# Performance work log

Measured on AMD Instinct MI355X. Metric: run time of the kernel, lower is better.

The kernel has to match this reference:

```python
import jax, jax.numpy as jnp
import numpy as np

N_NODES = 100000


def gcn_layer(x, src, dst, W, b):
    """PyG GCNConv: add self-loops, symmetric deg normalization, XW then scatter-add."""
    n = x.shape[0]
    loop = jnp.arange(n, dtype=src.dtype)
    s = jnp.concatenate([src, loop])
    d = jnp.concatenate([dst, loop])
    # degree of target nodes (includes self-loop)
    deg = jax.ops.segment_sum(jnp.ones_like(d, dtype=x.dtype), d, num_segments=n)
    dinv = jnp.where(deg > 0, jax.lax.rsqrt(deg), 0.0)
    norm = dinv[s] * dinv[d]                      # [E+N]
    h = x @ W                                     # [N, out]
    msg = h[s] * norm[:, None]                    # [E+N, out]
    out = jax.ops.segment_sum(msg, d, num_segments=n) + b
    return out


def setup_inputs() -> dict:
    key = jax.random.key(0)
    k1, k2, k3, k4 = jax.random.split(key, 4)
    d_in, d_hid, d_out = 256, 256, 128
    E = 3200000
    x = jax.random.normal(k1, (N_NODES, d_in), dtype=jnp.float32)
    edge_index = jax.random.randint(k2, (2, E), 0, N_NODES, dtype=jnp.int64)
    # glorot-style init for GCN weights
    W1 = jax.random.normal(k3, (d_in, d_hid), dtype=jnp.float32) / np.sqrt(d_in)
    b1 = jnp.zeros((d_hid,), dtype=jnp.float32)
    W2 = jax.random.normal(k4, (d_hid, d_out), dtype=jnp.float32) / np.sqrt(d_hid)
    b2 = jnp.zeros((d_out,), dtype=jnp.float32)
    return {"x": x, "W1": W1, "b1": b1, "W2": W2, "b2": b2, "edge_index": edge_index}


def reference(x, W1, b1, W2, b2, edge_index):
    src, dst = edge_index[0], edge_index[1]
    h = jax.nn.relu(gcn_layer(x, src, dst, W1, b1))
    out = jax.nn.relu(gcn_layer(h, src, dst, W2, b2))
    return out
```

## Files before the change

kernel.cpp:

```cpp
#include <hip/hip_runtime.h>


typedef short          s16x8 __attribute__((ext_vector_type(8)));
typedef float          f32x4 __attribute__((ext_vector_type(4)));
typedef float          f32x2 __attribute__((ext_vector_type(2)));
typedef unsigned short u16x8 __attribute__((ext_vector_type(8)));
typedef unsigned short u16x4 __attribute__((ext_vector_type(4)));

__device__ __forceinline__ float bf2f(unsigned short u) {
  union { unsigned int i; float f; } x; x.i = ((unsigned int)u) << 16; return x.f;
}
__device__ __forceinline__ unsigned short f2bf(float f) {
  union { float f; unsigned int i; } x; x.f = f;
  unsigned int r = x.i + 0x7FFFu + ((x.i >> 16) & 1u);
  return (unsigned short)(r >> 16);
}
__device__ __forceinline__ void acc2(f32x2& a, unsigned int pair) {
  union { unsigned int u; float f; } lo, hi;
  lo.u = pair << 16;
  hi.u = pair & 0xFFFF0000u;
  f32x2 v = {lo.f, hi.f};
  a += v;
}


#define NBUCK_PAD 1024
#define BIN_CHUNK 32768

__global__ __launch_bounds__(256) void k_hist(const int* __restrict__ dst,
                                              int* __restrict__ bcnt, int E) {
  __shared__ int h[NBUCK_PAD];
  int t = threadIdx.x;
  for (int i = t; i < NBUCK_PAD; i += 256) h[i] = 0;
  __syncthreads();
  int n4 = E >> 2;
  int stride = gridDim.x * 256;
  const int4* d4 = (const int4*)dst;
  for (int e = blockIdx.x * 256 + t; e < n4; e += stride) {
    int4 v = d4[e];
    atomicAdd(&h[v.x >> 7], 1);
    atomicAdd(&h[v.y >> 7], 1);
    atomicAdd(&h[v.z >> 7], 1);
    atomicAdd(&h[v.w >> 7], 1);
  }
  if (blockIdx.x == 0) {
    for (int e = n4 * 4 + t; e < E; e += 256) atomicAdd(&h[dst[e] >> 7], 1);
  }
  __syncthreads();
  for (int i = t; i < NBUCK_PAD; i += 256) {
    int v = h[i];
    if (v) atomicAdd(bcnt + i, v);
  }
}

__global__ void k_bscan(const int* __restrict__ bcnt, int* __restrict__ bptr,
                        int* __restrict__ bcur, int* __restrict__ rowptr, int M, int E) {
  __shared__ int sh[NBUCK_PAD];
  int t = threadIdx.x;
  int v = bcnt[t];
  sh[t] = v; __syncthreads();
  int x = v;
  for (int off = 1; off < NBUCK_PAD; off <<= 1) {
    int y = (t >= off) ? sh[t - off] : 0;
    __syncthreads();
    x += y; sh[t] = x;
    __syncthreads();
  }
  bptr[t] = x - v;
  bcur[t] = x - v;
  if (t == NBUCK_PAD - 1) bptr[NBUCK_PAD] = x;
  if (t == 0) rowptr[M] = E;
}

__global__ __launch_bounds__(256) void k_bin(const int* __restrict__ src,
                                             const int* __restrict__ dst,
                                             int* __restrict__ bcur,
                                             unsigned int* __restrict__ binned, int E) {
  __shared__ int hist[NBUCK_PAD];
  __shared__ int base[NBUCK_PAD];
  int t = threadIdx.x;
  int e0 = blockIdx.x * BIN_CHUNK;
  int e1 = min(e0 + BIN_CHUNK, E);
  for (int i = t; i < NBUCK_PAD; i += 256) hist[i] = 0;
  __syncthreads();
  for (int e = e0 + t; e < e1; e += 256) atomicAdd(&hist[dst[e] >> 7], 1);
  __syncthreads();
  for (int i = t; i < NBUCK_PAD; i += 256) {
    int h = hist[i];
    base[i] = h ? atomicAdd(bcur + i, h) : 0;
    hist[i] = 0;
  }
  __syncthreads();
  for (int e = e0 + t; e < e1; e += 256) {
    int d = dst[e], s = src[e];
    int b = d >> 7;
    int p = base[b] + atomicAdd(&hist[b], 1);
    binned[p] = ((unsigned)(d & 127) << 17) | (unsigned)s;
  }
}

__global__ __launch_bounds__(256) void k_csr(const unsigned int* __restrict__ binned,
                                             const int* __restrict__ bptr,
                                             int* __restrict__ rowptr,
                                             float* __restrict__ dinv,
                                             int* __restrict__ col, int M) {
  __shared__ int deg[128];
  __shared__ int sc[128];
  __shared__ int cur[128];
  int b = blockIdx.x, t = threadIdx.x;
  int n0 = b << 7;
  int nn = min(128, M - n0);
  int e0 = bptr[b], e1 = bptr[b + 1];
  if (t < 128) deg[t] = 0;
  __syncthreads();
  for (int e = e0 + t; e < e1; e += 256) atomicAdd(&deg[(binned[e] >> 17) & 127], 1);
  __syncthreads();
  if (t < 128) sc[t] = deg[t];
  __syncthreads();
  for (int off = 1; off < 128; off <<= 1) {
    int y = 0;
    if (t < 128 && t >= off) y = sc[t - off];
    __syncthreads();
    if (t < 128) sc[t] += y;
    __syncthreads();
  }
  if (t < nn) {
    int excl = sc[t] - deg[t];
    rowptr[n0 + t] = e0 + excl;
    dinv[n0 + t] = rsqrtf((float)(deg[t] + 1));
    cur[t] = excl;
  }
  __syncthreads();
  for (int e = e0 + t; e < e1; e += 256) {
    unsigned v = binned[e];
    int dl = (v >> 17) & 127;
    int p = e0 + atomicAdd(&cur[dl], 1);
    col[p] = (int)(v & 0x1FFFFu);
  }
}


__global__ void k_cvt_w(const float* __restrict__ W1, const float* __restrict__ W2,
                        unsigned short* __restrict__ w1t, unsigned short* __restrict__ w2t) {
  int i = blockIdx.x * 256 + threadIdx.x;
  if (i < 256 * 256) {
    int k = i >> 8, n = i & 255;
    w1t[n * 256 + k] = f2bf(W1[i]);
  } else {
    int j = i - 256 * 256;
    if (j < 256 * 128) {
      int k = j >> 7, n = j & 127;
      w2t[n * 256 + k] = f2bf(W2[j]);
    }
  }
}


__device__ __forceinline__ int swz4(int row, int kc) { return kc ^ ((row & 3) << 3); }

__global__ __launch_bounds__(512) void k_gemm1(
    const float* __restrict__ X, const unsigned short* __restrict__ Bt,
    const float* __restrict__ dinv, unsigned short* __restrict__ G, int M) {
  const int K = 256;
  __shared__ short lA[128 * 32];
  __shared__ short lB[256 * 32];
  int tid = threadIdx.x;
  int wid = tid >> 6, lane = tid & 63;
  int wm = wid >> 2, wn = wid & 3;
  int l15 = lane & 15;
  int lkg = (lane >> 4) * 8;
  int bm = blockIdx.x * 128;

  f32x4 acc[4][4] = {};

  for (int kt = 0; kt < 8; ++kt) {
    int k0 = kt * 32;
    __syncthreads();
#pragma unroll
    for (int h = 0; h < 2; ++h) {
      int cid = tid + h * 512;
      int r = cid >> 3, c4 = (cid & 7) * 4;
      int gr = bm + r;
      float4 v = {0.f, 0.f, 0.f, 0.f};
      if (gr < M) v = *(const float4*)(X + (size_t)gr * K + k0 + c4);
      u16x4 o; o[0] = f2bf(v.x); o[1] = f2bf(v.y); o[2] = f2bf(v.z); o[3] = f2bf(v.w);
      *(u16x4*)(&lA[r * 32 + swz4(r, c4)]) = o;
    }
#pragma unroll
    for (int h = 0; h < 2; ++h) {
      int cid = tid + h * 512;
      int n = cid >> 2, kc = (cid & 3) * 8;
      s16x8 v = *(const s16x8*)(Bt + (size_t)n * K + k0 + kc);
      *(s16x8*)(&lB[n * 32 + swz4(n, kc)]) = v;
    }
    __syncthreads();

    s16x8 af[4], bfr[4];
#pragma unroll
    for (int mi = 0; mi < 4; ++mi) {
      int r = wm * 64 + mi * 16 + l15;
      af[mi] = *(const s16x8*)(&lA[r * 32 + swz4(r, lkg)]);
    }
#pragma unroll
    for (int ni = 0; ni < 4; ++ni) {
      int c = wn * 64 + ni * 16 + l15;
      bfr[ni] = *(const s16x8*)(&lB[c * 32 + swz4(c, lkg)]);
    }
#pragma unroll
    for (int mi = 0; mi < 4; ++mi)
#pragma unroll
      for (int ni = 0; ni < 4; ++ni)
        acc[mi][ni] = __builtin_amdgcn_mfma_f32_16x16x32_bf16(af[mi], bfr[ni], acc[mi][ni], 0, 0, 0);
  }

#pragma unroll
  for (int mi = 0; mi < 4; ++mi) {
    int mrow0 = bm + wm * 64 + mi * 16 + (lane >> 4) * 4;
#pragma unroll
    for (int j = 0; j < 4; ++j) {
      int m = mrow0 + j;
      if (m < M) {
        float dv = dinv[m];
#pragma unroll
        for (int ni = 0; ni < 4; ++ni)
          G[(size_t)m * 256 + wn * 64 + ni * 16 + l15] = f2bf(acc[mi][ni][j] * dv);
      }
    }
  }
}


__global__ __launch_bounds__(512) void k_gemm2(
    const unsigned short* __restrict__ A, const unsigned short* __restrict__ Bt,
    const float* __restrict__ dinv, unsigned short* __restrict__ G, int M) {
  const int K = 256;
  __shared__ short lA[128 * 32];
  __shared__ short lB[128 * 32];
  int tid = threadIdx.x;
  int wid = tid >> 6, lane = tid & 63;
  int wm = wid >> 2, wn = wid & 3;
  int l15 = lane & 15;
  int lkg = (lane >> 4) * 8;
  int bm = blockIdx.x * 128;

  f32x4 acc[4][2] = {};

  for (int kt = 0; kt < 8; ++kt) {
    int k0 = kt * 32;
    __syncthreads();
    {
      int r = tid >> 2, kc = (tid & 3) * 8;
      int gr = bm + r;
      s16x8 v = {0, 0, 0, 0, 0, 0, 0, 0};
      if (gr < M) v = *(const s16x8*)(A + (size_t)gr * K + k0 + kc);
      *(s16x8*)(&lA[r * 32 + swz4(r, kc)]) = v;
    }
    {
      int n = tid >> 2, kc = (tid & 3) * 8;
      s16x8 v = *(const s16x8*)(Bt + (size_t)n * K + k0 + kc);
      *(s16x8*)(&lB[n * 32 + swz4(n, kc)]) = v;
    }
    __syncthreads();

    s16x8 af[4], bfr[2];
#pragma unroll
    for (int mi = 0; mi < 4; ++mi) {
      int r = wm * 64 + mi * 16 + l15;
      af[mi] = *(const s16x8*)(&lA[r * 32 + swz4(r, lkg)]);
    }
#pragma unroll
    for (int ni = 0; ni < 2; ++ni) {
      int c = wn * 32 + ni * 16 + l15;
      bfr[ni] = *(const s16x8*)(&lB[c * 32 + swz4(c, lkg)]);
    }
#pragma unroll
    for (int mi = 0; mi < 4; ++mi)
#pragma unroll
      for (int ni = 0; ni < 2; ++ni)
        acc[mi][ni] = __builtin_amdgcn_mfma_f32_16x16x32_bf16(af[mi], bfr[ni], acc[mi][ni], 0, 0, 0);
  }

#pragma unroll
  for (int mi = 0; mi < 4; ++mi) {
    int mrow0 = bm + wm * 64 + mi * 16 + (lane >> 4) * 4;
#pragma unroll
    for (int j = 0; j < 4; ++j) {
      int m = mrow0 + j;
      if (m < M) {
        float dv = dinv[m];
#pragma unroll
        for (int ni = 0; ni < 2; ++ni)
          G[(size_t)m * 128 + wn * 32 + ni * 16 + l15] = f2bf(acc[mi][ni][j] * dv);
      }
    }
  }
}


__global__ __launch_bounds__(256) void k_agg256(
    const unsigned short* __restrict__ G, const int* __restrict__ rowptr,
    const int* __restrict__ col, const float* __restrict__ dinv,
    const float* __restrict__ bias, unsigned short* __restrict__ H, int M) {
  int lane = threadIdx.x & 63;
  int v = (blockIdx.x << 2) + (threadIdx.x >> 6);
  if (v >= M) return;
  int slot = lane >> 5;
  int l32 = lane & 31;
  int boff = l32 * 16;
  const char* Gb = (const char*)G;
  f32x2 a[4] = {};
  if (slot == 0) {
    uint4 w = *(const uint4*)(Gb + (((unsigned)v) << 9) + boff);
    acc2(a[0], w.x); acc2(a[1], w.y); acc2(a[2], w.z); acc2(a[3], w.w);
  }
  int jb = rowptr[v], je = rowptr[v + 1];
  int j = jb;
  for (; j + 4 <= je; j += 4) {
    unsigned u0 = (unsigned)col[j + slot];
    unsigned u1 = (unsigned)col[j + 2 + slot];
    uint4 w0 = *(const uint4*)(Gb + (u0 << 9) + boff);
    uint4 w1 = *(const uint4*)(Gb + (u1 << 9) + boff);
    acc2(a[0], w0.x); acc2(a[1], w0.y); acc2(a[2], w0.z); acc2(a[3], w0.w);
    acc2(a[0], w1.x); acc2(a[1], w1.y); acc2(a[2], w1.z); acc2(a[3], w1.w);
  }
  for (; j + 2 <= je; j += 2) {
    unsigned u = (unsigned)col[j + slot];
    uint4 w = *(const uint4*)(Gb + (u << 9) + boff);
    acc2(a[0], w.x); acc2(a[1], w.y); acc2(a[2], w.z); acc2(a[3], w.w);
  }
  if (j < je && slot == 0) {
    unsigned u = (unsigned)col[j];
    uint4 w = *(const uint4*)(Gb + (u << 9) + boff);
    acc2(a[0], w.x); acc2(a[1], w.y); acc2(a[2], w.z); acc2(a[3], w.w);
  }
#pragma unroll
  for (int k = 0; k < 4; ++k) {
    a[k].x += __shfl_xor(a[k].x, 32, 64);
    a[k].y += __shfl_xor(a[k].y, 32, 64);
  }
  if (slot == 0) {
    float dv = dinv[v];
    const float* bp = bias + l32 * 8;
    u16x8 o;
#pragma unroll
    for (int k = 0; k < 4; ++k) {
      o[2 * k]     = f2bf(fmaxf(fmaf(dv, a[k].x, bp[2 * k]),     0.f));
      o[2 * k + 1] = f2bf(fmaxf(fmaf(dv, a[k].y, bp[2 * k + 1]), 0.f));
    }
    *(u16x8*)(H + (size_t)v * 256 + l32 * 8) = o;
  }
}


__global__ __launch_bounds__(256) void k_agg128(
    const unsigned short* __restrict__ G, const int* __restrict__ rowptr,
    const int* __restrict__ col, const float* __restrict__ dinv,
    const float* __restrict__ bias, float* __restrict__ Out, int M) {
  int lane = threadIdx.x & 63;
  int v = (blockIdx.x << 2) + (threadIdx.x >> 6);
  if (v >= M) return;
  int slot = lane >> 4;
  int l16 = lane & 15;
  int boff = l16 * 16;
  const char* Gb = (const char*)G;
  f32x2 a[4] = {};
  if (slot == 0) {
    uint4 w = *(const uint4*)(Gb + (((unsigned)v) << 8) + boff);
    acc2(a[0], w.x); acc2(a[1], w.y); acc2(a[2], w.z); acc2(a[3], w.w);
  }
  int jb = rowptr[v], je = rowptr[v + 1];
  int j = jb;
  for (; j + 8 <= je; j += 8) {
    unsigned u0 = (unsigned)col[j + slot];
    unsigned u1 = (unsigned)col[j + 4 + slot];
    uint4 w0 = *(const uint4*)(Gb + (u0 << 8) + boff);
    uint4 w1 = *(const uint4*)(Gb + (u1 << 8) + boff);
    acc2(a[0], w0.x); acc2(a[1], w0.y); acc2(a[2], w0.z); acc2(a[3], w0.w);
    acc2(a[0], w1.x); acc2(a[1], w1.y); acc2(a[2], w1.z); acc2(a[3], w1.w);
  }
  for (; j + 4 <= je; j += 4) {
    unsigned u = (unsigned)col[j + slot];
    uint4 w = *(const uint4*)(Gb + (u << 8) + boff);
    acc2(a[0], w.x); acc2(a[1], w.y); acc2(a[2], w.z); acc2(a[3], w.w);
  }
  int rem = je - j;
  if (slot < rem) {
    unsigned u = (unsigned)col[j + slot];
    uint4 w = *(const uint4*)(Gb + (u << 8) + boff);
    acc2(a[0], w.x); acc2(a[1], w.y); acc2(a[2], w.z); acc2(a[3], w.w);
  }
#pragma unroll
  for (int k = 0; k < 4; ++k) {
    a[k].x += __shfl_xor(a[k].x, 16, 64);
    a[k].y += __shfl_xor(a[k].y, 16, 64);
    a[k].x += __shfl_xor(a[k].x, 32, 64);
    a[k].y += __shfl_xor(a[k].y, 32, 64);
  }
  if (slot == 0) {
    float dv = dinv[v];
    const float* bp = bias + l16 * 8;
    float4 r0, r1;
    r0.x = fmaxf(fmaf(dv, a[0].x, bp[0]), 0.f);
    r0.y = fmaxf(fmaf(dv, a[0].y, bp[1]), 0.f);
    r0.z = fmaxf(fmaf(dv, a[1].x, bp[2]), 0.f);
    r0.w = fmaxf(fmaf(dv, a[1].y, bp[3]), 0.f);
    r1.x = fmaxf(fmaf(dv, a[2].x, bp[4]), 0.f);
    r1.y = fmaxf(fmaf(dv, a[2].y, bp[5]), 0.f);
    r1.z = fmaxf(fmaf(dv, a[3].x, bp[6]), 0.f);
    r1.w = fmaxf(fmaf(dv, a[3].y, bp[7]), 0.f);
    float* op = Out + (size_t)v * 128 + l16 * 8;
    *(float4*)op = r0;
    *(float4*)(op + 4) = r1;
  }
}


extern "C" void kernel_launch(void* const* d_in, const int* in_sizes, int n_in,
                              void* d_out, int out_size, void* d_ws, size_t ws_size,
                              hipStream_t stream) {
  const float* x  = (const float*)d_in[0];
  const float* W1 = (const float*)d_in[1];
  const float* b1 = (const float*)d_in[2];
  const float* W2 = (const float*)d_in[3];
  const float* b2 = (const float*)d_in[4];
  const int*   ei = (const int*)d_in[5];

  const int D_IN = 256, D_HID = 256, D_OUT = 128;
  const int M = in_sizes[0] / D_IN;
  const int E = in_sizes[5] / 2;
  const int* src = ei;
  const int* dst = ei + E;

  char* p = (char*)d_ws;
  auto alloc = [&](size_t bytes) { void* r = (void*)p; p += (bytes + 255) & ~(size_t)255; return r; };
  float* dinv = (float*)alloc((size_t)M * 4);
  int* rowptr = (int*)alloc((size_t)(M + 1) * 4);
  int* bcnt   = (int*)alloc(NBUCK_PAD * 4);
  int* bptr   = (int*)alloc((NBUCK_PAD + 1) * 4);
  int* bcur   = (int*)alloc(NBUCK_PAD * 4);
  int* colx   = (int*)alloc((size_t)E * 4);
  unsigned short* w1t = (unsigned short*)alloc((size_t)D_HID * D_IN * 2);
  unsigned short* w2t = (unsigned short*)alloc((size_t)D_OUT * D_HID * 2);
  unsigned short* g1  = (unsigned short*)alloc((size_t)M * D_HID * 2);
  unsigned short* hid = (unsigned short*)alloc((size_t)M * D_HID * 2);
  unsigned short* g2  = (unsigned short*)alloc((size_t)M * D_OUT * 2);
  unsigned int* binned = (unsigned int*)g1;

  int nbuck = (M + 127) >> 7;
  int nbin  = (E + BIN_CHUNK - 1) / BIN_CHUNK;
  int nb4   = (M + 3) / 4;

  hipMemsetAsync(bcnt, 0, NBUCK_PAD * 4, stream);
  k_hist <<<104, 256, 0, stream>>>(dst, bcnt, E);
  k_bscan<<<1, NBUCK_PAD, 0, stream>>>(bcnt, bptr, bcur, rowptr, M, E);
  k_bin  <<<nbin, 256, 0, stream>>>(src, dst, bcur, binned, E);
  k_csr  <<<nbuck, 256, 0, stream>>>(binned, bptr, rowptr, dinv, colx, M);

  k_cvt_w<<<(256 * 256 + 256 * 128 + 255) / 256, 256, 0, stream>>>(W1, W2, w1t, w2t);

  k_gemm1 <<<nbuck, 512, 0, stream>>>(x, w1t, dinv, g1, M);
  k_agg256<<<nb4, 256, 0, stream>>>(g1, rowptr, colx, dinv, b1, hid, M);
  k_gemm2 <<<nbuck, 512, 0, stream>>>(hid, w2t, dinv, g2, M);
  k_agg128<<<nb4, 256, 0, stream>>>(g2, rowptr, colx, dinv, b2, (float*)d_out, M);
}
```

Baseline: 552.1 us.

## Shrink GEMM tiles to 64 rows, add nontemporal memory ops, smaller bin chunk

Both GEMMs now use 64-row tiles with 256-thread blocks and a 2x2 wave layout, each wave covering more output columns. This doubles the grid size for better occupancy across CUs. Streaming loads of column indices and stores of GEMM/aggregation outputs now use nontemporal hints to limit cache pollution, and the edge binning chunk is reduced so more blocks are launched. Risks: the B tile is reloaded more often per output row, and the nontemporal stores may evict data the next kernel wants to read from cache.

```diff
diff --git a/kernel.cpp b/kernel.cpp
--- a/kernel.cpp
+++ b/kernel.cpp
@@ -25,7 +25,7 @@
 
 
 #define NBUCK_PAD 1024
-#define BIN_CHUNK 32768
+#define BIN_CHUNK 8192
 
 __global__ __launch_bounds__(256) void k_hist(const int* __restrict__ dst,
                                               int* __restrict__ bcnt, int E) {
@@ -158,27 +158,27 @@
 
 __device__ __forceinline__ int swz4(int row, int kc) { return kc ^ ((row & 3) << 3); }
 
-__global__ __launch_bounds__(512) void k_gemm1(
+__global__ __launch_bounds__(256) void k_gemm1(
     const float* __restrict__ X, const unsigned short* __restrict__ Bt,
     const float* __restrict__ dinv, unsigned short* __restrict__ G, int M) {
   const int K = 256;
-  __shared__ short lA[128 * 32];
+  __shared__ short lA[64 * 32];
   __shared__ short lB[256 * 32];
   int tid = threadIdx.x;
   int wid = tid >> 6, lane = tid & 63;
-  int wm = wid >> 2, wn = wid & 3;
+  int wm = wid >> 1, wn = wid & 1;
   int l15 = lane & 15;
   int lkg = (lane >> 4) * 8;
-  int bm = blockIdx.x * 128;
-
-  f32x4 acc[4][4] = {};
+  int bm = blockIdx.x * 64;
+
+  f32x4 acc[2][8] = {};
 
   for (int kt = 0; kt < 8; ++kt) {
     int k0 = kt * 32;
     __syncthreads();
 #pragma unroll
     for (int h = 0; h < 2; ++h) {
-      int cid = tid + h * 512;
+      int cid = tid + h * 256;
       int r = cid >> 3, c4 = (cid & 7) * 4;
       int gr = bm + r;
       float4 v = {0.f, 0.f, 0.f, 0.f};
@@ -187,63 +187,64 @@
       *(u16x4*)(&lA[r * 32 + swz4(r, c4)]) = o;
     }
 #pragma unroll
-    for (int h = 0; h < 2; ++h) {
-      int cid = tid + h * 512;
+    for (int h = 0; h < 4; ++h) {
+      int cid = tid + h * 256;
       int n = cid >> 2, kc = (cid & 3) * 8;
       s16x8 v = *(const s16x8*)(Bt + (size_t)n * K + k0 + kc);
       *(s16x8*)(&lB[n * 32 + swz4(n, kc)]) = v;
     }
     __syncthreads();
 
-    s16x8 af[4], bfr[4];
-#pragma unroll
-    for (int mi = 0; mi < 4; ++mi) {
-      int r = wm * 64 + mi * 16 + l15;
+    s16x8 af[2], bfr[8];
+#pragma unroll
+    for (int mi = 0; mi < 2; ++mi) {
+      int r = wm * 32 + mi * 16 + l15;
       af[mi] = *(const s16x8*)(&lA[r * 32 + swz4(r, lkg)]);
     }
 #pragma unroll
-    for (int ni = 0; ni < 4; ++ni) {
-      int c = wn * 64 + ni * 16 + l15;
+    for (int ni = 0; ni < 8; ++ni) {
+      int c = wn * 128 + ni * 16 + l15;
       bfr[ni] = *(const s16x8*)(&lB[c * 32 + swz4(c, lkg)]);
     }
 #pragma unroll
-    for (int mi = 0; mi < 4; ++mi)
-#pragma unroll
-      for (int ni = 0; ni < 4; ++ni)
+    for (int mi = 0; mi < 2; ++mi)
+#pragma unroll
+      for (int ni = 0; ni < 8; ++ni)
         acc[mi][ni] = __builtin_amdgcn_mfma_f32_16x16x32_bf16(af[mi], bfr[ni], acc[mi][ni], 0, 0, 0);
   }
 
 #pragma unroll
-  for (int mi = 0; mi < 4; ++mi) {
-    int mrow0 = bm + wm * 64 + mi * 16 + (lane >> 4) * 4;
+  for (int mi = 0; mi < 2; ++mi) {
+    int mrow0 = bm + wm * 32 + mi * 16 + (lane >> 4) * 4;
 #pragma unroll
     for (int j = 0; j < 4; ++j) {
       int m = mrow0 + j;
       if (m < M) {
         float dv = dinv[m];
 #pragma unroll
-        for (int ni = 0; ni < 4; ++ni)
-          G[(size_t)m * 256 + wn * 64 + ni * 16 + l15] = f2bf(acc[mi][ni][j] * dv);
+        for (int ni = 0; ni < 8; ++ni)
+          __builtin_nontemporal_store(f2bf(acc[mi][ni][j] * dv),
+                                      G + (size_t)m * 256 + wn * 128 + ni * 16 + l15);
       }
     }
   }
 }
 
 
-__global__ __launch_bounds__(512) void k_gemm2(
+__global__ __launch_bounds__(256) void k_gemm2(
     const unsigned short* __restrict__ A, const unsigned short* __restrict__ Bt,
     const float* __restrict__ dinv, unsigned short* __restrict__ G, int M) {
   const int K = 256;
-  __shared__ short lA[128 * 32];
+  __shared__ short lA[64 * 32];
   __shared__ short lB[128 * 32];
   int tid = threadIdx.x;
   int wid = tid >> 6, lane = tid & 63;
-  int wm = wid >> 2, wn = wid & 3;
+  int wm = wid >> 1, wn = wid & 1;
   int l15 = lane & 15;
   int lkg = (lane >> 4) * 8;
-  int bm = blockIdx.x * 128;
-
-  f32x4 acc[4][2] = {};
+  int bm = blockIdx.x * 64;
+
+  f32x4 acc[2][4] = {};
 
   for (int kt = 0; kt < 8; ++kt) {
     int k0 = kt * 32;
@@ -255,42 +256,45 @@
       if (gr < M) v = *(const s16x8*)(A + (size_t)gr * K + k0 + kc);
       *(s16x8*)(&lA[r * 32 + swz4(r, kc)]) = v;
     }
-    {
-      int n = tid >> 2, kc = (tid & 3) * 8;
+#pragma unroll
+    for (int h = 0; h < 2; ++h) {
+      int cid = tid + h * 256;
+      int n = cid >> 2, kc = (cid & 3) * 8;
       s16x8 v = *(const s16x8*)(Bt + (size_t)n * K + k0 + kc);
       *(s16x8*)(&lB[n * 32 + swz4(n, kc)]) = v;
     }
     __syncthreads();
 
-    s16x8 af[4], bfr[2];
-#pragma unroll
-    for (int mi = 0; mi < 4; ++mi) {
-      int r = wm * 64 + mi * 16 + l15;
+    s16x8 af[2], bfr[4];
+#pragma unroll
+    for (int mi = 0; mi < 2; ++mi) {
+      int r = wm * 32 + mi * 16 + l15;
       af[mi] = *(const s16x8*)(&lA[r * 32 + swz4(r, lkg)]);
     }
 #pragma unroll
-    for (int ni = 0; ni < 2; ++ni) {
-      int c = wn * 32 + ni * 16 + l15;
+    for (int ni = 0; ni < 4; ++ni) {
+      int c = wn * 64 + ni * 16 + l15;
       bfr[ni] = *(const s16x8*)(&lB[c * 32 + swz4(c, lkg)]);
     }
 #pragma unroll
-    for (int mi = 0; mi < 4; ++mi)
-#pragma unroll
-      for (int ni = 0; ni < 2; ++ni)
+    for (int mi = 0; mi < 2; ++mi)
+#pragma unroll
+      for (int ni = 0; ni < 4; ++ni)
         acc[mi][ni] = __builtin_amdgcn_mfma_f32_16x16x32_bf16(af[mi], bfr[ni], acc[mi][ni], 0, 0, 0);
   }
 
 #pragma unroll
-  for (int mi = 0; mi < 4; ++mi) {
-    int mrow0 = bm + wm * 64 + mi * 16 + (lane >> 4) * 4;
+  for (int mi = 0; mi < 2; ++mi) {
+    int mrow0 = bm + wm * 32 + mi * 16 + (lane >> 4) * 4;
 #pragma unroll
     for (int j = 0; j < 4; ++j) {
       int m = mrow0 + j;
       if (m < M) {
         float dv = dinv[m];
 #pragma unroll
-        for (int ni = 0; ni < 2; ++ni)
-          G[(size_t)m * 128 + wn * 32 + ni * 16 + l15] = f2bf(acc[mi][ni][j] * dv);
+        for (int ni = 0; ni < 4; ++ni)
+          __builtin_nontemporal_store(f2bf(acc[mi][ni][j] * dv),
+                                      G + (size_t)m * 128 + wn * 64 + ni * 16 + l15);
       }
     }
   }
@@ -316,20 +320,20 @@
   int jb = rowptr[v], je = rowptr[v + 1];
   int j = jb;
   for (; j + 4 <= je; j += 4) {
-    unsigned u0 = (unsigned)col[j + slot];
-    unsigned u1 = (unsigned)col[j + 2 + slot];
+    unsigned u0 = (unsigned)__builtin_nontemporal_load(col + j + slot);
+    unsigned u1 = (unsigned)__builtin_nontemporal_load(col + j + 2 + slot);
     uint4 w0 = *(const uint4*)(Gb + (u0 << 9) + boff);
     uint4 w1 = *(const uint4*)(Gb + (u1 << 9) + boff);
     acc2(a[0], w0.x); acc2(a[1], w0.y); acc2(a[2], w0.z); acc2(a[3], w0.w);
     acc2(a[0], w1.x); acc2(a[1], w1.y); acc2(a[2], w1.z); acc2(a[3], w1.w);
   }
   for (; j + 2 <= je; j += 2) {
-    unsigned u = (unsigned)col[j + slot];
+    unsigned u = (unsigned)__builtin_nontemporal_load(col + j + slot);
     uint4 w = *(const uint4*)(Gb + (u << 9) + boff);
     acc2(a[0], w.x); acc2(a[1], w.y); acc2(a[2], w.z); acc2(a[3], w.w);
   }
   if (j < je && slot == 0) {
-    unsigned u = (unsigned)col[j];
+    unsigned u = (unsigned)__builtin_nontemporal_load(col + j);
     uint4 w = *(const uint4*)(Gb + (u << 9) + boff);
     acc2(a[0], w.x); acc2(a[1], w.y); acc2(a[2], w.z); acc2(a[3], w.w);
   }
@@ -347,7 +351,7 @@
       o[2 * k]     = f2bf(fmaxf(fmaf(dv, a[k].x, bp[2 * k]),     0.f));
       o[2 * k + 1] = f2bf(fmaxf(fmaf(dv, a[k].y, bp[2 * k + 1]), 0.f));
     }
-    *(u16x8*)(H + (size_t)v * 256 + l32 * 8) = o;
+    __builtin_nontemporal_store(o, (u16x8*)(H + (size_t)v * 256 + l32 * 8));
   }
 }
 
@@ -371,21 +375,21 @@
   int jb = rowptr[v], je = rowptr[v + 1];
   int j = jb;
   for (; j + 8 <= je; j += 8) {
-    unsigned u0 = (unsigned)col[j + slot];
-    unsigned u1 = (unsigned)col[j + 4 + slot];
+    unsigned u0 = (unsigned)__builtin_nontemporal_load(col + j + slot);
+    unsigned u1 = (unsigned)__builtin_nontemporal_load(col + j + 4 + slot);
     uint4 w0 = *(const uint4*)(Gb + (u0 << 8) + boff);
     uint4 w1 = *(const uint4*)(Gb + (u1 << 8) + boff);
     acc2(a[0], w0.x); acc2(a[1], w0.y); acc2(a[2], w0.z); acc2(a[3], w0.w);
     acc2(a[0], w1.x); acc2(a[1], w1.y); acc2(a[2], w1.z); acc2(a[3], w1.w);
   }
   for (; j + 4 <= je; j += 4) {
-    unsigned u = (unsigned)col[j + slot];
+    unsigned u = (unsigned)__builtin_nontemporal_load(col + j + slot);
     uint4 w = *(const uint4*)(Gb + (u << 8) + boff);
     acc2(a[0], w.x); acc2(a[1], w.y); acc2(a[2], w.z); acc2(a[3], w.w);
   }
   int rem = je - j;
   if (slot < rem) {
-    unsigned u = (unsigned)col[j + slot];
+    unsigned u = (unsigned)__builtin_nontemporal_load(col + j + slot);
     uint4 w = *(const uint4*)(Gb + (u << 8) + boff);
     acc2(a[0], w.x); acc2(a[1], w.y); acc2(a[2], w.z); acc2(a[3], w.w);
   }
@@ -399,18 +403,18 @@
   if (slot == 0) {
     float dv = dinv[v];
     const float* bp = bias + l16 * 8;
-    float4 r0, r1;
-    r0.x = fmaxf(fmaf(dv, a[0].x, bp[0]), 0.f);
-    r0.y = fmaxf(fmaf(dv, a[0].y, bp[1]), 0.f);
-    r0.z = fmaxf(fmaf(dv, a[1].x, bp[2]), 0.f);
-    r0.w = fmaxf(fmaf(dv, a[1].y, bp[3]), 0.f);
-    r1.x = fmaxf(fmaf(dv, a[2].x, bp[4]), 0.f);
-    r1.y = fmaxf(fmaf(dv, a[2].y, bp[5]), 0.f);
-    r1.z = fmaxf(fmaf(dv, a[3].x, bp[6]), 0.f);
-    r1.w = fmaxf(fmaf(dv, a[3].y, bp[7]), 0.f);
+    f32x4 r0, r1;
+    r0[0] = fmaxf(fmaf(dv, a[0].x, bp[0]), 0.f);
+    r0[1] = fmaxf(fmaf(dv, a[0].y, bp[1]), 0.f);
+    r0[2] = fmaxf(fmaf(dv, a[1].x, bp[2]), 0.f);
+    r0[3] = fmaxf(fmaf(dv, a[1].y, bp[3]), 0.f);
+    r1[0] = fmaxf(fmaf(dv, a[2].x, bp[4]), 0.f);
+    r1[1] = fmaxf(fmaf(dv, a[2].y, bp[5]), 0.f);
+    r1[2] = fmaxf(fmaf(dv, a[3].x, bp[6]), 0.f);
+    r1[3] = fmaxf(fmaf(dv, a[3].y, bp[7]), 0.f);
     float* op = Out + (size_t)v * 128 + l16 * 8;
-    *(float4*)op = r0;
-    *(float4*)(op + 4) = r1;
+    __builtin_nontemporal_store(r0, (f32x4*)op);
+    __builtin_nontemporal_store(r1, (f32x4*)(op + 4));
   }
 }
 
@@ -449,6 +453,7 @@
   int nbuck = (M + 127) >> 7;
   int nbin  = (E + BIN_CHUNK - 1) / BIN_CHUNK;
   int nb4   = (M + 3) / 4;
+  int ngm   = (M + 63) / 64;
 
   hipMemsetAsync(bcnt, 0, NBUCK_PAD * 4, stream);
   k_hist <<<104, 256, 0, stream>>>(dst, bcnt, E);
@@ -458,8 +463,8 @@
 
   k_cvt_w<<<(256 * 256 + 256 * 128 + 255) / 256, 256, 0, stream>>>(W1, W2, w1t, w2t);
 
-  k_gemm1 <<<nbuck, 512, 0, stream>>>(x, w1t, dinv, g1, M);
+  k_gemm1 <<<ngm, 256, 0, stream>>>(x, w1t, dinv, g1, M);
   k_agg256<<<nb4, 256, 0, stream>>>(g1, rowptr, colx, dinv, b1, hid, M);
-  k_gemm2 <<<nbuck, 512, 0, stream>>>(hid, w2t, dinv, g2, M);
+  k_gemm2 <<<ngm, 256, 0, stream>>>(hid, w2t, dinv, g2, M);
   k_agg128<<<nb4, 256, 0, stream>>>(g2, rowptr, colx, dinv, b2, (float*)d_out, M);
 }
```

Measured after the change: 506.4 us. 1.09x faster.
